# Kernel optimization log

Hardware: AMD Instinct MI355X
Metric: run time of the kernel (lower is better)

## Reference

```python
import jax, jax.numpy as jnp
import numpy as np

# static config (Phi-3-like with GQA)
B, S, H, HKV, D, BS = 2, 2048, 32, 8, 128, 64
HID = H * D
NB = B * (S // BS)  # total cache blocks
THETA = 10000.0


def rotate_half(x):
    x1, x2 = jnp.split(x, 2, axis=-1)
    return jnp.concatenate([-x2, x1], axis=-1)


def rope_cos_sin(positions):
    # positions: [T] int -> cos/sin [T, D]
    inv_freq = 1.0 / (THETA ** (jnp.arange(0, D, 2, dtype=jnp.float32) / D))
    freqs = positions.astype(jnp.float32)[:, None] * inv_freq[None, :]
    emb = jnp.concatenate([freqs, freqs], axis=-1)
    return jnp.cos(emb), jnp.sin(emb)


def setup_inputs() -> dict:
    key = jax.random.key(0)
    k1, k2, k3 = jax.random.split(key, 3)
    T = B * S
    hidden_states = jax.random.normal(k1, (T, HID), dtype=jnp.float32)
    w_qkv = jax.random.normal(k2, ((H + 2 * HKV) * D, HID), dtype=jnp.float32) * 0.02
    w_o = jax.random.normal(k3, (HID, H * D), dtype=jnp.float32) * 0.02
    k_cache = jnp.zeros((NB, BS, HKV, D), dtype=jnp.float32)
    v_cache = jnp.zeros((NB, BS, HKV, D), dtype=jnp.float32)
    position_ids = jnp.tile(jnp.arange(S, dtype=jnp.int32), B)  # per-token positions (prefill)
    block_offsets = jnp.arange(NB, dtype=jnp.int32).reshape(B, S // BS)
    return dict(hidden_states=hidden_states, w_qkv=w_qkv, w_o=w_o,
                k_cache=k_cache, v_cache=v_cache, position_ids=position_ids,
                block_offsets=block_offsets, window_size=1024)


def reference(hidden_states, w_qkv, w_o, k_cache, v_cache, position_ids, block_offsets, window_size):
    # fused qkv projection + split
    qkv = hidden_states @ w_qkv.T  # [T, (H+2*HKV)*D]
    q, k, v = jnp.split(qkv, [H * D, H * D + HKV * D], axis=-1)
    q = q.reshape(-1, H, D)
    k = k.reshape(-1, HKV, D)
    v = v.reshape(-1, HKV, D)

    # rotary embedding on flattened tokens
    cos, sin = rope_cos_sin(position_ids)  # [T, D]
    cos, sin = cos[:, None, :], sin[:, None, :]
    q = q * cos + rotate_half(q) * sin
    k = k * cos + rotate_half(k) * sin

    # fill paged KV cache: token t of seq b -> block block_offsets[b, t//BS], slot t%BS
    flat_blocks = block_offsets.reshape(-1)  # [NB]
    k_blk = k.reshape(NB, BS, HKV, D)
    v_blk = v.reshape(NB, BS, HKV, D)
    k_cache = k_cache.at[flat_blocks].set(k_blk)
    v_cache = v_cache.at[flat_blocks].set(v_blk)

    # paged attention: gather per-sequence K/V through the block table
    k_seq = k_cache[block_offsets].reshape(B, S, HKV, D)
    v_seq = v_cache[block_offsets].reshape(B, S, HKV, D)

    G = H // HKV  # query heads per kv head (GQA)
    qh = q.reshape(B, S, HKV, G, D)
    scale = 1.0 / jnp.sqrt(jnp.float32(D))
    scores = jnp.einsum('bshgd,bthd->bhgst', qh, k_seq) * scale  # [B,HKV,G,S,S]

    # causal + sliding-window mask: j <= i and i - j < window_size
    i = jnp.arange(S)[:, None]
    j = jnp.arange(S)[None, :]
    mask = (j <= i) & ((i - j) < window_size)  # [S,S]
    scores = jnp.where(mask[None, None, None], scores, jnp.finfo(scores.dtype).min)
    probs = jax.nn.softmax(scores, axis=-1)

    out = jnp.einsum('bhgst,bthd->bshgd', probs, v_seq)  # [B,S,HKV,G,D]
    out = out.reshape(B * S, H * D)
    return out @ w_o.T  # [T, HID]
```

## Files before the change

kernel.cpp:

```cpp
#include <hip/hip_runtime.h>
#include <hip/hip_bf16.h>
#include <stdint.h>

typedef unsigned short u16;
typedef __attribute__((ext_vector_type(8))) short short8;
typedef __attribute__((ext_vector_type(8))) unsigned short u16x8;
typedef __attribute__((ext_vector_type(4))) float f32x4;

#define B_    2
#define S_    2048
#define H_    32
#define HKV_  8
#define D_    128
#define HID_  4096
#define QKVW_ 6144

__device__ __forceinline__ u16 f2bf(float f){
  uint32_t b = __builtin_bit_cast(uint32_t, f);
  b += 0x7FFFu + ((b >> 16) & 1u);
  return (u16)(b >> 16);
}
__device__ __forceinline__ float bf2f(u16 h){
  uint32_t b = ((uint32_t)h) << 16;
  return __builtin_bit_cast(float, b);
}
__device__ __forceinline__ u16 bfc(float f){
  __hip_bfloat16 h = __float2bfloat16(f);
  return __builtin_bit_cast(u16, h);
}

__device__ __forceinline__ void gload16(const u16* g, u16* l){
  __builtin_amdgcn_global_load_lds((const __attribute__((address_space(1))) void*)g,
                                   (__attribute__((address_space(3))) void*)l, 16, 0, 0);
}

__global__ void cvt_kernel(const float* __restrict__ src, u16* __restrict__ dst, int n4){
  int i = blockIdx.x * blockDim.x + threadIdx.x;
  int stride = gridDim.x * blockDim.x;
  for (; i < n4; i += stride){
    float4 v = reinterpret_cast<const float4*>(src)[i];
    union { u16 u[4]; unsigned long long ll; } o;
    o.u[0] = f2bf(v.x); o.u[1] = f2bf(v.y); o.u[2] = f2bf(v.z); o.u[3] = f2bf(v.w);
    reinterpret_cast<unsigned long long*>(dst)[i] = o.ll;
  }
}

__global__ void rope_table_kernel(float2* __restrict__ tab){
  int idx = blockIdx.x * blockDim.x + threadIdx.x;
  if (idx >= S_ * 64) return;
  int pos = idx >> 6, p = idx & 63;
  float inv = powf(10000.0f, -(float)p / 64.0f);
  float ang = (float)pos * inv;
  tab[idx] = make_float2(cosf(ang), sinf(ang));
}

__global__ void rope_apply_kernel(u16* __restrict__ qkv, const int* __restrict__ pos_ids,
                                  const float2* __restrict__ tab){
  const float QS = 0.08838834764831845f * 1.4426950408889634f;
  int t = blockIdx.x;
  int pos = pos_ids[t];
  const float2* tb = tab + pos * 64;
  u16* row = qkv + (size_t)t * QKVW_;
  for (int it = threadIdx.x; it < (H_ + HKV_) * 64; it += 256){
    int hh = it >> 6, p = it & 63;
    int base = (hh < H_) ? hh * D_ : HID_ + (hh - H_) * D_;
    float sc = (hh < H_) ? QS : 1.0f;
    float x1 = bf2f(row[base + p]);
    float x2 = bf2f(row[base + 64 + p]);
    float2 cs = tb[p];
    row[base + p]      = f2bf((x1 * cs.x - x2 * cs.y) * sc);
    row[base + 64 + p] = f2bf((x2 * cs.x + x1 * cs.y) * sc);
  }
}

template<int CF>
__global__ __launch_bounds__(256) void gemm_bt(const u16* __restrict__ A, const u16* __restrict__ B,
                                               void* __restrict__ Cv, int M, int N, int K){
  __shared__ u16 As[128*64];
  __shared__ u16 Bs[128*64];
  const int tid  = threadIdx.x;
  const int wave = tid >> 6, lane = tid & 63;
  const int hi = lane >> 4, lo = lane & 15;
  const int bn = blockIdx.x, bm = blockIdx.y;
  const int wm = (wave >> 1) * 64, wn = (wave & 1) * 64;
  f32x4 acc[4][4] = {};

  const u16* ap[4]; const u16* bp[4];
  u16* lA[4]; u16* lB[4];
  #pragma unroll
  for (int p = 0; p < 4; p++){
    int e   = p*2048 + wave*512 + lane*8;
    int row = e >> 6;
    int cs  = ((e >> 3) & 7) ^ (row & 7);
    ap[p] = A + (size_t)(bm*128 + row) * K + cs*8;
    bp[p] = B + (size_t)(bn*128 + row) * K + cs*8;
    lA[p] = &As[p*2048 + wave*512];
    lB[p] = &Bs[p*2048 + wave*512];
  }
  const int sw = lo & 7;
  const int nk = K >> 6;
  for (int t = 0; t < nk; t++){
    #pragma unroll
    for (int p = 0; p < 4; p++){
      gload16(ap[p], lA[p]);
      gload16(bp[p], lB[p]);
      ap[p] += 64; bp[p] += 64;
    }
    __syncthreads();
    #pragma unroll
    for (int kk = 0; kk < 2; kk++){
      short8 af[4], bf[4];
      int sz = ((kk*4 + hi) ^ sw) * 8;
      #pragma unroll
      for (int mt = 0; mt < 4; mt++) af[mt] = *(const short8*)&As[(wm + mt*16 + lo)*64 + sz];
      #pragma unroll
      for (int nt = 0; nt < 4; nt++) bf[nt] = *(const short8*)&Bs[(wn + nt*16 + lo)*64 + sz];
      #pragma unroll
      for (int mt = 0; mt < 4; mt++)
        #pragma unroll
        for (int nt = 0; nt < 4; nt++)
          acc[mt][nt] = __builtin_amdgcn_mfma_f32_16x16x32_bf16(af[mt], bf[nt], acc[mt][nt], 0, 0, 0);
    }
    __syncthreads();
  }
  #pragma unroll
  for (int mt = 0; mt < 4; mt++){
    int row = bm*128 + wm + mt*16 + 4*hi;
    #pragma unroll
    for (int nt = 0; nt < 4; nt++){
      int col = bn*128 + wn + nt*16 + lo;
      #pragma unroll
      for (int r = 0; r < 4; r++){
        if (CF == 0) ((u16*)Cv)[(size_t)(row + r)*N + col] = f2bf(acc[mt][nt][r]);
        else         ((float*)Cv)[(size_t)(row + r)*N + col] = acc[mt][nt][r];
      }
    }
  }
}

__global__ __launch_bounds__(256) void attn_kernel(const u16* __restrict__ qkv, u16* __restrict__ out,
                                                   const int* __restrict__ winp){
  const int h = blockIdx.x, qt = blockIdx.y, b = blockIdx.z;
  const int hkv = h >> 2;
  const int q0 = qt * 64;
  const int tid = threadIdx.x, wave = tid >> 6, lane = tid & 63;
  const int lo = lane & 15, hi = lane >> 4;
  const int win = winp[0];

  __shared__ u16 Ks[2][64*128];
  __shared__ uint32_t VT[2][128*36];
  __shared__ u16 Pl[4][16*72];

  const int qw = q0 + wave*16;
  short8 qf[4];
  {
    const u16* qp = qkv + (size_t)(b*S_ + qw + lo)*QKVW_ + h*D_ + hi*8;
    #pragma unroll
    for (int c = 0; c < 4; c++) qf[c] = *(const short8*)(qp + c*32);
  }

  f32x4 accO[8] = {};
  float m_r = -3.0e38f, l_r = 0.0f;

  int js = q0 - (win - 1); if (js < 0) js = 0; js &= ~63;
  const int nt = (q0 + 64 - js) >> 6;

  const u16* Kg = qkv + (size_t)HID_ + hkv*D_;
  const u16* Vg = qkv + (size_t)HID_ + HKV_*D_ + hkv*D_;
  const int jp = tid & 31, d0 = (tid >> 5) * 16;

  const u16* ksrc[4];
  #pragma unroll
  for (int p = 0; p < 4; p++){
    int e = p*256 + tid;
    int row = e >> 4;
    int ss = (e & 15) ^ (row & 7);
    ksrc[p] = Kg + (size_t)(b*S_ + js + row)*QKVW_ + ss*8;
  }
  const u16* vsrc = Vg + (size_t)(b*S_ + js + 2*jp)*QKVW_ + d0;

  u16x8 vr0, vr1, vr2, vr3;
  {
    #pragma unroll
    for (int p = 0; p < 4; p++) gload16(ksrc[p], &Ks[0][p*2048 + wave*512]);
    vr0 = *(const u16x8*)(vsrc);
    vr1 = *(const u16x8*)(vsrc + 8);
    vr2 = *(const u16x8*)(vsrc + QKVW_);
    vr3 = *(const u16x8*)(vsrc + QKVW_ + 8);
    #pragma unroll
    for (int i = 0; i < 8; i++){
      VT[0][(d0+i)*36 + jp]   = (uint32_t)vr0[i] | ((uint32_t)vr2[i] << 16);
      VT[0][(d0+8+i)*36 + jp] = (uint32_t)vr1[i] | ((uint32_t)vr3[i] << 16);
    }
  }
  __syncthreads();

  for (int t = 0; t < nt; t++){
    const int jc = js + t*64;
    const int cur = t & 1, nxt = cur ^ 1;
    const bool more = (t + 1 < nt);
    if (more){
      const size_t adv = (size_t)(t+1) * 64 * QKVW_;
      #pragma unroll
      for (int p = 0; p < 4; p++) gload16(ksrc[p] + adv, &Ks[nxt][p*2048 + wave*512]);
      const u16* vp = vsrc + adv;
      vr0 = *(const u16x8*)(vp);
      vr1 = *(const u16x8*)(vp + 8);
      vr2 = *(const u16x8*)(vp + QKVW_);
      vr3 = *(const u16x8*)(vp + QKVW_ + 8);
    }
    if (jc <= qw + 15 && jc + 63 >= qw - win + 1){
      f32x4 s[4] = {};
      #pragma unroll
      for (int jt = 0; jt < 4; jt++)
        #pragma unroll
        for (int c = 0; c < 4; c++){
          short8 kf = *(const short8*)&Ks[cur][(jt*16+lo)*128 + (((c*4+hi) ^ (lo & 7)) * 8)];
          s[jt] = __builtin_amdgcn_mfma_f32_16x16x32_bf16(kf, qf[c], s[jt], 0, 0, 0);
        }
      const int qa = qw + lo;
      const bool fullv = (jc + 63 <= qw) && (jc >= qw + 16 - win);
      if (!fullv){
        #pragma unroll
        for (int jt = 0; jt < 4; jt++)
          #pragma unroll
          for (int r = 0; r < 4; r++){
            int j = jc + jt*16 + 4*hi + r;
            if (j > qa || qa - j >= win) s[jt][r] = -3.0e38f;
          }
      }
      float mx = s[0][0];
      #pragma unroll
      for (int jt = 0; jt < 4; jt++)
        #pragma unroll
        for (int r = 0; r < 4; r++) mx = fmaxf(mx, s[jt][r]);
      mx = fmaxf(mx, __shfl_xor(mx, 16));
      mx = fmaxf(mx, __shfl_xor(mx, 32));
      if (__any(mx > m_r + 8.0f)){
        float mn = fmaxf(m_r, mx);
        float al = exp2f(m_r - mn);
        m_r = mn; l_r *= al;
        float a0 = __shfl(al, 4*hi+0), a1 = __shfl(al, 4*hi+1);
        float a2 = __shfl(al, 4*hi+2), a3 = __shfl(al, 4*hi+3);
        #pragma unroll
        for (int dt = 0; dt < 8; dt++){
          accO[dt][0] *= a0; accO[dt][1] *= a1;
          accO[dt][2] *= a2; accO[dt][3] *= a3;
        }
      }
      float ps = 0.f;
      #pragma unroll
      for (int jt = 0; jt < 4; jt++){
        float p0, p1, p2, p3;
        if (fullv){
          p0 = exp2f(s[jt][0] - m_r); p1 = exp2f(s[jt][1] - m_r);
          p2 = exp2f(s[jt][2] - m_r); p3 = exp2f(s[jt][3] - m_r);
        } else {
          p0 = s[jt][0] > -1e37f ? exp2f(s[jt][0] - m_r) : 0.f;
          p1 = s[jt][1] > -1e37f ? exp2f(s[jt][1] - m_r) : 0.f;
          p2 = s[jt][2] > -1e37f ? exp2f(s[jt][2] - m_r) : 0.f;
          p3 = s[jt][3] > -1e37f ? exp2f(s[jt][3] - m_r) : 0.f;
        }
        ps += (p0 + p1) + (p2 + p3);
        uint32_t w0 = (uint32_t)bfc(p0) | ((uint32_t)bfc(p1) << 16);
        uint32_t w1 = (uint32_t)bfc(p2) | ((uint32_t)bfc(p3) << 16);
        *(uint64_t*)&Pl[wave][lo*72 + jt*16 + 4*hi] = (uint64_t)w0 | ((uint64_t)w1 << 32);
      }
      ps += __shfl_xor(ps, 16);
      ps += __shfl_xor(ps, 32);
      l_r += ps;
      short8 pa0 = *(const short8*)&Pl[wave][lo*72 + hi*8];
      short8 pa1 = *(const short8*)&Pl[wave][lo*72 + 32 + hi*8];
      const u16* VT16 = (const u16*)&VT[cur][0];
      #pragma unroll
      for (int dt = 0; dt < 8; dt++){
        short8 vf0 = *(const short8*)&VT16[(dt*16+lo)*72 + hi*8];
        short8 vf1 = *(const short8*)&VT16[(dt*16+lo)*72 + 32 + hi*8];
        accO[dt] = __builtin_amdgcn_mfma_f32_16x16x32_bf16(pa0, vf0, accO[dt], 0, 0, 0);
        accO[dt] = __builtin_amdgcn_mfma_f32_16x16x32_bf16(pa1, vf1, accO[dt], 0, 0, 0);
      }
    }
    if (more){
      #pragma unroll
      for (int i = 0; i < 8; i++){
        VT[nxt][(d0+i)*36 + jp]   = (uint32_t)vr0[i] | ((uint32_t)vr2[i] << 16);
        VT[nxt][(d0+8+i)*36 + jp] = (uint32_t)vr1[i] | ((uint32_t)vr3[i] << 16);
      }
      __syncthreads();
    }
  }
  #pragma unroll
  for (int r = 0; r < 4; r++){
    float lr = __shfl(l_r, 4*hi + r);
    float invl = 1.0f / lr;
    int trow = b*S_ + qw + 4*hi + r;
    #pragma unroll
    for (int dt = 0; dt < 8; dt++)
      out[(size_t)trow*HID_ + h*D_ + dt*16 + lo] = f2bf(accO[dt][r] * invl);
  }
}

extern "C" void kernel_launch(void* const* d_in, const int* in_sizes, int n_in,
                              void* d_out, int out_size, void* d_ws, size_t ws_size,
                              hipStream_t stream) {
  const float* hs   = (const float*)d_in[0];
  const float* wqkv = (const float*)d_in[1];
  const float* wo   = (const float*)d_in[2];
  const int* pos  = (const int*)d_in[5];
  const int* winp = (const int*)d_in[7];
  float* out = (float*)d_out;

  u16* hsb = (u16*)d_ws;
  u16* wqb = hsb + (size_t)HID_*HID_;
  u16* wob = wqb + (size_t)QKVW_*HID_;
  u16* qkv = wob + (size_t)HID_*HID_;
  u16* att = qkv + (size_t)(B_*S_)*QKVW_;
  float2* tab = (float2*)(att + (size_t)(B_*S_)*HID_);

  cvt_kernel<<<2048, 256, 0, stream>>>(hs,   hsb, HID_*HID_/4);
  cvt_kernel<<<2048, 256, 0, stream>>>(wqkv, wqb, QKVW_*HID_/4);
  cvt_kernel<<<2048, 256, 0, stream>>>(wo,   wob, HID_*HID_/4);
  rope_table_kernel<<<(S_*64 + 255)/256, 256, 0, stream>>>(tab);
  gemm_bt<0><<<dim3(QKVW_/128, (B_*S_)/128), 256, 0, stream>>>(hsb, wqb, (void*)qkv, B_*S_, QKVW_, HID_);
  rope_apply_kernel<<<B_*S_, 256, 0, stream>>>(qkv, pos, tab);
  attn_kernel<<<dim3(H_, S_/64, B_), 256, 0, stream>>>(qkv, att, winp);
  gemm_bt<1><<<dim3(HID_/128, (B_*S_)/128), 256, 0, stream>>>(att, wob, (void*)out, B_*S_, HID_, HID_);
}
```

Baseline: 587.7 us.

## Use 256x256 double-buffered GEMM tiles with XCD-aware block remapping

The bf16 GEMM is rewritten to use 512-thread workgroups computing 256x256 output tiles. The LDS buffers for A and B are double-buffered so the next K-slice is prefetched while MFMAs run on the current one. Blockidx is remapped so that neighbouring tiles land on the same XCD, and MFMA phases are wrapped in s_setprio. The larger tile raises data reuse and hides global-load latency, at the cost of 128KB of LDS, fewer resident blocks per CU, and coarser wave quantization (384 and 256 blocks).

Result: slower. 691.5 us (+17.7%).

```diff
diff --git a/kernel.cpp b/kernel.cpp
--- a/kernel.cpp
+++ b/kernel.cpp
@@ -73,66 +73,145 @@
   }
 }
 
+#define MFMA_(a, b, c) __builtin_amdgcn_mfma_f32_16x16x32_bf16((a), (b), (c), 0, 0, 0)
+
 template<int CF>
-__global__ __launch_bounds__(256) void gemm_bt(const u16* __restrict__ A, const u16* __restrict__ B,
-                                               void* __restrict__ Cv, int M, int N, int K){
-  __shared__ u16 As[128*64];
-  __shared__ u16 Bs[128*64];
-  const int tid  = threadIdx.x;
-  const int wave = tid >> 6, lane = tid & 63;
-  const int hi = lane >> 4, lo = lane & 15;
-  const int bn = blockIdx.x, bm = blockIdx.y;
-  const int wm = (wave >> 1) * 64, wn = (wave & 1) * 64;
-  f32x4 acc[4][4] = {};
-
-  const u16* ap[4]; const u16* bp[4];
-  u16* lA[4]; u16* lB[4];
+__global__ __launch_bounds__(512, 2) void gemm_bt(const u16* __restrict__ A, const u16* __restrict__ B,
+                                                  void* __restrict__ Cv, int M, int N, int K, int nbn){
+  __shared__ u16 As[2][256*64];
+  __shared__ u16 Bs[2][256*64];
+  const int tid = threadIdx.x;
+  const int wave = tid >> 6, lane = tid & 63, lo = lane & 15, hi = lane >> 4;
+  const int wr = wave >> 2, wc = wave & 3;
+  const int slotBase = lo & 7;
+
+  const int nwg = gridDim.x;
+  const int bid = blockIdx.x;
+  const int cpx = nwg >> 3;
+  const int wg = (bid & 7) * cpx + (bid >> 3);
+  const int bm = wg / nbn, bn = wg - bm * nbn;
+
+  f32x4 acc[8][4] = {};
+
+  const int rbase = tid >> 3;
+  const int cs = (tid & 7) ^ (rbase & 7);
+  const u16* ap = A + ((size_t)(bm*256 + rbase))*K + cs*8;
+  const u16* bp = B + ((size_t)(bn*256 + rbase))*K + cs*8;
+  const size_t pstride = (size_t)64 * K;
+  u16* const dA = &As[0][0] + wave*512;
+  u16* const dB = &Bs[0][0] + wave*512;
+
   #pragma unroll
   for (int p = 0; p < 4; p++){
-    int e   = p*2048 + wave*512 + lane*8;
-    int row = e >> 6;
-    int cs  = ((e >> 3) & 7) ^ (row & 7);
-    ap[p] = A + (size_t)(bm*128 + row) * K + cs*8;
-    bp[p] = B + (size_t)(bn*128 + row) * K + cs*8;
-    lA[p] = &As[p*2048 + wave*512];
-    lB[p] = &Bs[p*2048 + wave*512];
-  }
-  const int sw = lo & 7;
+    gload16(ap + p*pstride, dA + p*4096);
+    gload16(bp + p*pstride, dB + p*4096);
+  }
+  asm volatile("s_waitcnt vmcnt(0)" ::: "memory");
+  __builtin_amdgcn_s_barrier();
+
   const int nk = K >> 6;
-  for (int t = 0; t < nk; t++){
-    #pragma unroll
-    for (int p = 0; p < 4; p++){
-      gload16(ap[p], lA[p]);
-      gload16(bp[p], lB[p]);
-      ap[p] += 64; bp[p] += 64;
-    }
-    __syncthreads();
-    #pragma unroll
-    for (int kk = 0; kk < 2; kk++){
-      short8 af[4], bf[4];
-      int sz = ((kk*4 + hi) ^ sw) * 8;
-      #pragma unroll
-      for (int mt = 0; mt < 4; mt++) af[mt] = *(const short8*)&As[(wm + mt*16 + lo)*64 + sz];
-      #pragma unroll
-      for (int nt = 0; nt < 4; nt++) bf[nt] = *(const short8*)&Bs[(wn + nt*16 + lo)*64 + sz];
-      #pragma unroll
-      for (int mt = 0; mt < 4; mt++)
-        #pragma unroll
-        for (int nt = 0; nt < 4; nt++)
-          acc[mt][nt] = __builtin_amdgcn_mfma_f32_16x16x32_bf16(af[mt], bf[nt], acc[mt][nt], 0, 0, 0);
-    }
-    __syncthreads();
-  }
+  for (int t = 0; t < nk; ++t){
+    const int cur = t & 1, nxt = cur ^ 1;
+    if (t + 1 < nk){
+      const u16* a2 = ap + (size_t)(t+1)*64;
+      const u16* b2 = bp + (size_t)(t+1)*64;
+      u16* da = dA + nxt*16384;
+      u16* db = dB + nxt*16384;
+      #pragma unroll
+      for (int p = 0; p < 4; p++){
+        gload16(a2 + p*pstride, da + p*4096);
+        gload16(b2 + p*pstride, db + p*4096);
+      }
+    }
+    const u16* Ac = &As[cur][0];
+    const u16* Bc = &Bs[cur][0];
+    short8 av[8], bv[4];
+
+    #pragma unroll
+    for (int mt = 0; mt < 4; mt++)
+      #pragma unroll
+      for (int kk = 0; kk < 2; kk++)
+        av[mt*2+kk] = *(const short8*)&Ac[(wr*128 + mt*16 + lo)*64 + (((kk*4+hi)^slotBase)*8)];
+    #pragma unroll
+    for (int nt = 0; nt < 2; nt++)
+      #pragma unroll
+      for (int kk = 0; kk < 2; kk++)
+        bv[nt*2+kk] = *(const short8*)&Bc[(wc*64 + nt*16 + lo)*64 + (((kk*4+hi)^slotBase)*8)];
+    __builtin_amdgcn_s_barrier();
+    __builtin_amdgcn_s_setprio(1);
+    #pragma unroll
+    for (int mt = 0; mt < 4; mt++)
+      #pragma unroll
+      for (int nt = 0; nt < 2; nt++)
+        #pragma unroll
+        for (int kk = 0; kk < 2; kk++)
+          acc[mt][nt] = MFMA_(av[mt*2+kk], bv[nt*2+kk], acc[mt][nt]);
+    __builtin_amdgcn_s_setprio(0);
+    __builtin_amdgcn_s_barrier();
+
+    #pragma unroll
+    for (int nt = 0; nt < 2; nt++)
+      #pragma unroll
+      for (int kk = 0; kk < 2; kk++)
+        bv[nt*2+kk] = *(const short8*)&Bc[(wc*64 + 32 + nt*16 + lo)*64 + (((kk*4+hi)^slotBase)*8)];
+    __builtin_amdgcn_s_barrier();
+    __builtin_amdgcn_s_setprio(1);
+    #pragma unroll
+    for (int mt = 0; mt < 4; mt++)
+      #pragma unroll
+      for (int nt = 0; nt < 2; nt++)
+        #pragma unroll
+        for (int kk = 0; kk < 2; kk++)
+          acc[mt][2+nt] = MFMA_(av[mt*2+kk], bv[nt*2+kk], acc[mt][2+nt]);
+    __builtin_amdgcn_s_setprio(0);
+    __builtin_amdgcn_s_barrier();
+
+    #pragma unroll
+    for (int mt = 0; mt < 4; mt++)
+      #pragma unroll
+      for (int kk = 0; kk < 2; kk++)
+        av[mt*2+kk] = *(const short8*)&Ac[(wr*128 + 64 + mt*16 + lo)*64 + (((kk*4+hi)^slotBase)*8)];
+    __builtin_amdgcn_s_barrier();
+    __builtin_amdgcn_s_setprio(1);
+    #pragma unroll
+    for (int mt = 0; mt < 4; mt++)
+      #pragma unroll
+      for (int nt = 0; nt < 2; nt++)
+        #pragma unroll
+        for (int kk = 0; kk < 2; kk++)
+          acc[4+mt][2+nt] = MFMA_(av[mt*2+kk], bv[nt*2+kk], acc[4+mt][2+nt]);
+    __builtin_amdgcn_s_setprio(0);
+    __builtin_amdgcn_s_barrier();
+
+    #pragma unroll
+    for (int nt = 0; nt < 2; nt++)
+      #pragma unroll
+      for (int kk = 0; kk < 2; kk++)
+        bv[nt*2+kk] = *(const short8*)&Bc[(wc*64 + nt*16 + lo)*64 + (((kk*4+hi)^slotBase)*8)];
+    __builtin_amdgcn_s_barrier();
+    __builtin_amdgcn_s_setprio(1);
+    #pragma unroll
+    for (int mt = 0; mt < 4; mt++)
+      #pragma unroll
+      for (int nt = 0; nt < 2; nt++)
+        #pragma unroll
+        for (int kk = 0; kk < 2; kk++)
+          acc[4+mt][nt] = MFMA_(av[mt*2+kk], bv[nt*2+kk], acc[4+mt][nt]);
+    __builtin_amdgcn_s_setprio(0);
+    asm volatile("s_waitcnt vmcnt(0)" ::: "memory");
+    __builtin_amdgcn_s_barrier();
+  }
+
   #pragma unroll
-  for (int mt = 0; mt < 4; mt++){
-    int row = bm*128 + wm + mt*16 + 4*hi;
-    #pragma unroll
-    for (int nt = 0; nt < 4; nt++){
-      int col = bn*128 + wn + nt*16 + lo;
+  for (int i = 0; i < 8; i++){
+    int row = bm*256 + wr*128 + (i>>2)*64 + (i&3)*16 + 4*hi;
+    #pragma unroll
+    for (int j = 0; j < 4; j++){
+      int col = bn*256 + wc*64 + (j>>1)*32 + (j&1)*16 + lo;
       #pragma unroll
       for (int r = 0; r < 4; r++){
-        if (CF == 0) ((u16*)Cv)[(size_t)(row + r)*N + col] = f2bf(acc[mt][nt][r]);
-        else         ((float*)Cv)[(size_t)(row + r)*N + col] = acc[mt][nt][r];
+        if (CF == 0) ((u16*)Cv)[(size_t)(row + r)*N + col] = f2bf(acc[i][j][r]);
+        else         ((float*)Cv)[(size_t)(row + r)*N + col] = acc[i][j][r];
       }
     }
   }
@@ -321,8 +400,8 @@
   cvt_kernel<<<2048, 256, 0, stream>>>(wqkv, wqb, QKVW_*HID_/4);
   cvt_kernel<<<2048, 256, 0, stream>>>(wo,   wob, HID_*HID_/4);
   rope_table_kernel<<<(S_*64 + 255)/256, 256, 0, stream>>>(tab);
-  gemm_bt<0><<<dim3(QKVW_/128, (B_*S_)/128), 256, 0, stream>>>(hsb, wqb, (void*)qkv, B_*S_, QKVW_, HID_);
+  gemm_bt<0><<<(B_*S_/256)*(QKVW_/256), 512, 0, stream>>>(hsb, wqb, (void*)qkv, B_*S_, QKVW_, HID_, QKVW_/256);
   rope_apply_kernel<<<B_*S_, 256, 0, stream>>>(qkv, pos, tab);
   attn_kernel<<<dim3(H_, S_/64, B_), 256, 0, stream>>>(qkv, att, winp);
-  gemm_bt<1><<<dim3(HID_/128, (B_*S_)/128), 256, 0, stream>>>(att, wob, (void*)out, B_*S_, HID_, HID_);
-}
+  gemm_bt<1><<<(B_*S_/256)*(HID_/256), 512, 0, stream>>>(att, wob, (void*)out, B_*S_, HID_, HID_, HID_/256);
+}
```

## Replace GEMM with 256x256-tile double-buffered pipelined kernel and XCD-aware block remap

Applied to the files above, without the earlier changes.

Both projection GEMMs move from a 128x128 tile, 256-thread kernel with a single LDS buffer to a 256x256 tile, 512-thread kernel. The new kernel double-buffers LDS, interleaves global prefetch of the next K tile with four MFMA phases using explicit waitcnt and barriers, and remaps block IDs across the 8 XCDs. The goal is to raise arithmetic intensity and hide global-load latency behind MFMA work. MFMA sections in the GEMM and attention kernels are wrapped in s_setprio raises. The larger tile uses 128 KB of LDS and many accumulator registers, which limits occupancy, and the grid shrinks to 384 or 256 workgroups.

New measurement: 577.9 us. About the same (-1.7%).

```diff
diff --git a/kernel.cpp b/kernel.cpp
--- a/kernel.cpp
+++ b/kernel.cpp
@@ -73,66 +73,123 @@
   }
 }
 
+#define MFMA_(a, b, c) __builtin_amdgcn_mfma_f32_16x16x32_bf16((a), (b), (c), 0, 0, 0)
+
 template<int CF>
-__global__ __launch_bounds__(256) void gemm_bt(const u16* __restrict__ A, const u16* __restrict__ B,
-                                               void* __restrict__ Cv, int M, int N, int K){
-  __shared__ u16 As[128*64];
-  __shared__ u16 Bs[128*64];
-  const int tid  = threadIdx.x;
-  const int wave = tid >> 6, lane = tid & 63;
-  const int hi = lane >> 4, lo = lane & 15;
-  const int bn = blockIdx.x, bm = blockIdx.y;
-  const int wm = (wave >> 1) * 64, wn = (wave & 1) * 64;
-  f32x4 acc[4][4] = {};
-
-  const u16* ap[4]; const u16* bp[4];
-  u16* lA[4]; u16* lB[4];
+__global__ __launch_bounds__(512, 2) void gemm256(const u16* __restrict__ A, const u16* __restrict__ B,
+                                                  void* __restrict__ Cv, int M, int N, int K, int nbn){
+  __shared__ u16 As[2][16384];
+  __shared__ u16 Bs[2][16384];
+  const int tid = threadIdx.x;
+  const int wave = tid >> 6, lane = tid & 63, lo = lane & 15, hi = lane >> 4;
+  const int wr = wave >> 2, wc = wave & 3;
+  const int sw = lo & 7;
+
+  const int nwg = gridDim.x, bid = blockIdx.x, cpx = nwg >> 3;
+  const int wg = (bid & 7) * cpx + (bid >> 3);
+  const int bm = wg / nbn, bn = wg - bm * nbn;
+
+  f32x4 acc[8][4] = {};
+
+  const int pr0 = tid >> 3;
+  const int sc0 = (tid & 7) ^ (pr0 & 7);
+  const u16* aS0 = A + ((size_t)(bm*256 + pr0      ))*K + sc0*8;
+  const u16* aS1 = A + ((size_t)(bm*256 + pr0 + 128))*K + sc0*8;
+  const u16* aS2 = A + ((size_t)(bm*256 + pr0 + 64 ))*K + sc0*8;
+  const u16* aS3 = A + ((size_t)(bm*256 + pr0 + 192))*K + sc0*8;
+  const u16* bS0 = B + ((size_t)(bn*256 + pr0      ))*K + sc0*8;
+  const u16* bS1 = B + ((size_t)(bn*256 + pr0 + 64 ))*K + sc0*8;
+  const u16* bS2 = B + ((size_t)(bn*256 + pr0 + 128))*K + sc0*8;
+  const u16* bS3 = B + ((size_t)(bn*256 + pr0 + 192))*K + sc0*8;
+  const int dOfs = tid * 8;
+
+  gload16(bS0, &Bs[0][dOfs]);        gload16(bS1, &Bs[0][4096 + dOfs]);
+  gload16(bS2, &Bs[0][8192 + dOfs]); gload16(bS3, &Bs[0][12288 + dOfs]);
+  gload16(aS0, &As[0][dOfs]);        gload16(aS1, &As[0][4096 + dOfs]);
+  gload16(aS2, &As[0][8192 + dOfs]); gload16(aS3, &As[0][12288 + dOfs]);
+  asm volatile("s_waitcnt vmcnt(0)" ::: "memory");
+  __builtin_amdgcn_s_barrier();
+
+  const int nk = K >> 6;
+  for (int t = 0; t < nk; ++t){
+    const int cur = t & 1, nxt = cur ^ 1;
+    const u16* Ac = &As[cur][0];
+    const u16* Bc = &Bs[cur][0];
+    u16* An = &As[nxt][0];
+    u16* Bn = &Bs[nxt][0];
+    const size_t ko = (size_t)(t + 1) * 64;
+    const bool more = (t + 1 < nk);
+    short8 avr[4], bvr[8];
+
+    #define RD_A(q) \
+      _Pragma("unroll") for (int mt = 0; mt < 2; mt++) \
+        _Pragma("unroll") for (int kk = 0; kk < 2; kk++){ \
+          int ra = wr*128 + (q)*32 + mt*16 + lo; \
+          int fo = ((ra & 63) << 6) + ((ra & 64) ? 8192 : 0) + ((ra & 128) ? 4096 : 0) \
+                 + ((((kk << 2) + hi) ^ sw) << 3); \
+          avr[mt*2 + kk] = *(const short8*)&Ac[fo]; \
+        }
+    #define DO_MFMA(q) \
+      __builtin_amdgcn_s_setprio(1); \
+      _Pragma("unroll") for (int mt = 0; mt < 2; mt++) \
+        _Pragma("unroll") for (int nt = 0; nt < 4; nt++) \
+          _Pragma("unroll") for (int kk = 0; kk < 2; kk++) \
+            acc[(q)*2 + mt][nt] = MFMA_(avr[mt*2 + kk], bvr[nt*2 + kk], acc[(q)*2 + mt][nt]); \
+      __builtin_amdgcn_s_setprio(0);
+
+    #pragma unroll
+    for (int nt = 0; nt < 4; nt++)
+      #pragma unroll
+      for (int kk = 0; kk < 2; kk++){
+        int rb = wc*64 + nt*16 + lo;
+        int fo = (rb << 6) + ((((kk << 2) + hi) ^ sw) << 3);
+        bvr[nt*2 + kk] = *(const short8*)&Bc[fo];
+      }
+    RD_A(0)
+    if (more){ gload16(bS0 + ko, Bn + dOfs); gload16(bS1 + ko, Bn + 4096 + dOfs); }
+    __builtin_amdgcn_s_barrier();
+    DO_MFMA(0)
+    __builtin_amdgcn_s_barrier();
+
+    RD_A(1)
+    if (more){
+      gload16(bS2 + ko, Bn + 8192 + dOfs); gload16(bS3 + ko, Bn + 12288 + dOfs);
+      asm volatile("s_waitcnt vmcnt(4)" ::: "memory");
+    } else {
+      asm volatile("s_waitcnt vmcnt(0)" ::: "memory");
+    }
+    __builtin_amdgcn_sched_barrier(0);
+    __builtin_amdgcn_s_barrier();
+    DO_MFMA(1)
+    __builtin_amdgcn_s_barrier();
+
+    RD_A(2)
+    if (more){ gload16(aS0 + ko, An + dOfs); gload16(aS1 + ko, An + 4096 + dOfs); }
+    __builtin_amdgcn_s_barrier();
+    DO_MFMA(2)
+    __builtin_amdgcn_s_barrier();
+
+    RD_A(3)
+    if (more){ gload16(aS2 + ko, An + 8192 + dOfs); gload16(aS3 + ko, An + 12288 + dOfs); }
+    asm volatile("s_waitcnt vmcnt(2)" ::: "memory");
+    __builtin_amdgcn_sched_barrier(0);
+    __builtin_amdgcn_s_barrier();
+    DO_MFMA(3)
+    __builtin_amdgcn_s_barrier();
+    #undef RD_A
+    #undef DO_MFMA
+  }
+
   #pragma unroll
-  for (int p = 0; p < 4; p++){
-    int e   = p*2048 + wave*512 + lane*8;
-    int row = e >> 6;
-    int cs  = ((e >> 3) & 7) ^ (row & 7);
-    ap[p] = A + (size_t)(bm*128 + row) * K + cs*8;
-    bp[p] = B + (size_t)(bn*128 + row) * K + cs*8;
-    lA[p] = &As[p*2048 + wave*512];
-    lB[p] = &Bs[p*2048 + wave*512];
-  }
-  const int sw = lo & 7;
-  const int nk = K >> 6;
-  for (int t = 0; t < nk; t++){
-    #pragma unroll
-    for (int p = 0; p < 4; p++){
-      gload16(ap[p], lA[p]);
-      gload16(bp[p], lB[p]);
-      ap[p] += 64; bp[p] += 64;
-    }
-    __syncthreads();
-    #pragma unroll
-    for (int kk = 0; kk < 2; kk++){
-      short8 af[4], bf[4];
-      int sz = ((kk*4 + hi) ^ sw) * 8;
-      #pragma unroll
-      for (int mt = 0; mt < 4; mt++) af[mt] = *(const short8*)&As[(wm + mt*16 + lo)*64 + sz];
-      #pragma unroll
-      for (int nt = 0; nt < 4; nt++) bf[nt] = *(const short8*)&Bs[(wn + nt*16 + lo)*64 + sz];
-      #pragma unroll
-      for (int mt = 0; mt < 4; mt++)
-        #pragma unroll
-        for (int nt = 0; nt < 4; nt++)
-          acc[mt][nt] = __builtin_amdgcn_mfma_f32_16x16x32_bf16(af[mt], bf[nt], acc[mt][nt], 0, 0, 0);
-    }
-    __syncthreads();
-  }
-  #pragma unroll
-  for (int mt = 0; mt < 4; mt++){
-    int row = bm*128 + wm + mt*16 + 4*hi;
+  for (int mtg = 0; mtg < 8; mtg++){
+    int row = bm*256 + wr*128 + mtg*16 + 4*hi;
     #pragma unroll
     for (int nt = 0; nt < 4; nt++){
-      int col = bn*128 + wn + nt*16 + lo;
+      int col = bn*256 + wc*64 + nt*16 + lo;
       #pragma unroll
       for (int r = 0; r < 4; r++){
-        if (CF == 0) ((u16*)Cv)[(size_t)(row + r)*N + col] = f2bf(acc[mt][nt][r]);
-        else         ((float*)Cv)[(size_t)(row + r)*N + col] = acc[mt][nt][r];
+        if (CF == 0) ((u16*)Cv)[(size_t)(row + r)*N + col] = f2bf(acc[mtg][nt][r]);
+        else         ((float*)Cv)[(size_t)(row + r)*N + col] = acc[mtg][nt][r];
       }
     }
   }
@@ -211,13 +268,15 @@
     }
     if (jc <= qw + 15 && jc + 63 >= qw - win + 1){
       f32x4 s[4] = {};
+      __builtin_amdgcn_s_setprio(1);
       #pragma unroll
       for (int jt = 0; jt < 4; jt++)
         #pragma unroll
         for (int c = 0; c < 4; c++){
           short8 kf = *(const short8*)&Ks[cur][(jt*16+lo)*128 + (((c*4+hi) ^ (lo & 7)) * 8)];
-          s[jt] = __builtin_amdgcn_mfma_f32_16x16x32_bf16(kf, qf[c], s[jt], 0, 0, 0);
+          s[jt] = MFMA_(kf, qf[c], s[jt]);
         }
+      __builtin_amdgcn_s_setprio(0);
       const int qa = qw + lo;
       const bool fullv = (jc + 63 <= qw) && (jc >= qw + 16 - win);
       if (!fullv){
@@ -272,13 +331,15 @@
       short8 pa0 = *(const short8*)&Pl[wave][lo*72 + hi*8];
       short8 pa1 = *(const short8*)&Pl[wave][lo*72 + 32 + hi*8];
       const u16* VT16 = (const u16*)&VT[cur][0];
+      __builtin_amdgcn_s_setprio(1);
       #pragma unroll
       for (int dt = 0; dt < 8; dt++){
         short8 vf0 = *(const short8*)&VT16[(dt*16+lo)*72 + hi*8];
         short8 vf1 = *(const short8*)&VT16[(dt*16+lo)*72 + 32 + hi*8];
-        accO[dt] = __builtin_amdgcn_mfma_f32_16x16x32_bf16(pa0, vf0, accO[dt], 0, 0, 0);
-        accO[dt] = __builtin_amdgcn_mfma_f32_16x16x32_bf16(pa1, vf1, accO[dt], 0, 0, 0);
-      }
+        accO[dt] = MFMA_(pa0, vf0, accO[dt]);
+        accO[dt] = MFMA_(pa1, vf1, accO[dt]);
+      }
+      __builtin_amdgcn_s_setprio(0);
     }
     if (more){
       #pragma unroll
@@ -321,8 +382,8 @@
   cvt_kernel<<<2048, 256, 0, stream>>>(wqkv, wqb, QKVW_*HID_/4);
   cvt_kernel<<<2048, 256, 0, stream>>>(wo,   wob, HID_*HID_/4);
   rope_table_kernel<<<(S_*64 + 255)/256, 256, 0, stream>>>(tab);
-  gemm_bt<0><<<dim3(QKVW_/128, (B_*S_)/128), 256, 0, stream>>>(hsb, wqb, (void*)qkv, B_*S_, QKVW_, HID_);
+  gemm256<0><<<(B_*S_/256)*(QKVW_/256), 512, 0, stream>>>(hsb, wqb, (void*)qkv, B_*S_, QKVW_, HID_, QKVW_/256);
   rope_apply_kernel<<<B_*S_, 256, 0, stream>>>(qkv, pos, tab);
   attn_kernel<<<dim3(H_, S_/64, B_), 256, 0, stream>>>(qkv, att, winp);
-  gemm_bt<1><<<dim3(HID_/128, (B_*S_)/128), 256, 0, stream>>>(att, wob, (void*)out, B_*S_, HID_, HID_);
-}
+  gemm256<1><<<(B_*S_/256)*(HID_/256), 512, 0, stream>>>(att, wob, (void*)out, B_*S_, HID_, HID_, HID_/256);
+}
```
